# Performance work log

Hardware: AMD Instinct MI355X
Metric: run time of the kernel (lower is better)

Reference implementation:

```python
import jax, jax.numpy as jnp
import numpy as np

INPUT_DIM = 1024
BOTTLENECK = 256
NUM_Q = 8
CODEBOOK = 1024
COMMIT_W = 0.25

def setup_inputs() -> dict:
    key = jax.random.key(0)
    ks = jax.random.split(key, 10)
    s_in = 1.0 / np.sqrt(INPUT_DIM)
    s_bn = 1.0 / np.sqrt(BOTTLENECK)
    return {
        'x': jax.random.normal(ks[0], (8, 2048, INPUT_DIM), jnp.float32),
        'W_e1': jax.random.uniform(ks[1], (INPUT_DIM, INPUT_DIM), jnp.float32, -s_in, s_in),
        'b_e1': jnp.zeros((INPUT_DIM,), jnp.float32),
        'W_e2': jax.random.uniform(ks[2], (INPUT_DIM, BOTTLENECK), jnp.float32, -s_in, s_in),
        'b_e2': jnp.zeros((BOTTLENECK,), jnp.float32),
        'codebooks': jax.random.normal(ks[3], (NUM_Q, CODEBOOK, BOTTLENECK), jnp.float32),
        'W_d1': jax.random.uniform(ks[4], (BOTTLENECK, INPUT_DIM), jnp.float32, -s_bn, s_bn),
        'b_d1': jnp.zeros((INPUT_DIM,), jnp.float32),
        'W_d2': jax.random.uniform(ks[5], (INPUT_DIM, INPUT_DIM), jnp.float32, -s_in, s_in),
        'b_d2': jnp.zeros((INPUT_DIM,), jnp.float32),
    }

def _gelu(x):
    return jax.nn.gelu(x, approximate=False)  # torch nn.GELU default = exact erf

def _rvq(z_flat, codebooks):
    # z_flat: [N, D]; codebooks: [Q, K, D]
    def step(res, cb):
        # squared L2 distances via expansion: [N, K]
        d2 = (jnp.sum(res * res, -1, keepdims=True)
              - 2.0 * res @ cb.T
              + jnp.sum(cb * cb, -1))
        idx = jnp.argmin(d2, axis=-1)                      # [N]
        q = jax.lax.stop_gradient(jnp.take(cb, idx, 0))    # [N, D] (EMA codebook: no grad)
        closs = jnp.mean((res - q) ** 2)
        return res - q, (idx, q, closs)
    _, (indices, qs, closses) = jax.lax.scan(step, z_flat, codebooks)
    q_total = jnp.sum(qs, axis=0)
    # straight-through estimator
    quantized = z_flat + jax.lax.stop_gradient(q_total - z_flat)
    commitment = COMMIT_W * jnp.mean(closses)
    return quantized, indices, commitment

def reference(x, W_e1, b_e1, W_e2, b_e2, codebooks, W_d1, b_d1, W_d2, b_d2):
    lead = x.shape[:-1]
    z = _gelu(x @ W_e1 + b_e1) @ W_e2 + b_e2               # [..., BOTTLENECK]
    zf = z.reshape(-1, BOTTLENECK)
    qf, indices, commitment = _rvq(zf, codebooks)
    quantized = qf.reshape(*lead, BOTTLENECK)
    indices = indices.reshape(NUM_Q, *lead)
    reconstructed = _gelu(quantized @ W_d1 + b_d1) @ W_d2 + b_d2
    return z, quantized, indices, reconstructed, commitment
```

## Files before the change

### kernel.cpp

```cpp
#include <hip/hip_runtime.h>
#include <math.h>

#define NROWS 16384
#define DIN   1024
#define DBN   256
#define NQ    8
#define NCODE 1024
#define MARGIN 2.0f

#define OFF_Z    0
#define OFF_Q    4194304
#define OFF_IDX  8388608
#define OFF_REC  8519680
#define OFF_COM  25296896

typedef __attribute__((ext_vector_type(8))) short short8v;
typedef __attribute__((ext_vector_type(4))) float f32x4;

__device__ __forceinline__ float gelu_f(float x) {
  return 0.5f * x * (1.0f + erff(x * 0.70710678118654752440f));
}

__device__ __forceinline__ ushort f2b(float x) {
  unsigned u = __float_as_uint(x);
  unsigned r = u + 0x7FFF + ((u >> 16) & 1);
  return (ushort)(r >> 16);
}
__device__ __forceinline__ float b2f(ushort u) {
  return __uint_as_float((unsigned)u << 16);
}
__device__ __forceinline__ void split3(float v, ushort& s1, ushort& s2, ushort& s3) {
  s1 = f2b(v);
  const float r1 = v - b2f(s1);
  s2 = f2b(r1);
  const float r2 = r1 - b2f(s2);
  s3 = f2b(r2);
}

template<bool GELU, int NB, int OUT>
__global__ __launch_bounds__(256) void gemm6(
    const float* __restrict__ Af,
    const ushort* __restrict__ B1, const ushort* __restrict__ B2,
    const ushort* __restrict__ B3,
    const float* __restrict__ bias,
    float* __restrict__ C0, float* __restrict__ C1, ushort* __restrict__ Ob,
    int N, int K)
{
  constexpr int BN = NB * 32;
  __shared__ char lds[24576 + BN * 192];
  char* ldsA = lds;
  char* ldsB = lds + 24576;
  const int tid = threadIdx.x;
  const int bm = blockIdx.x * 128;
  const int bn = blockIdx.y * BN;
  const int lane = tid & 63;
  const int wid = tid >> 6;
  const int wr = wid >> 1, wc = wid & 1;

  const int srow = tid >> 1, skh = tid & 1;
  const float* Ap = Af + (size_t)(bm + srow) * K + skh * 16;
  const int abase = srow * 192;
  const int aswz = (srow & 7) << 4;

  f32x4 acc[4][NB];
  #pragma unroll
  for (int m = 0; m < 4; ++m)
    #pragma unroll
    for (int n = 0; n < NB; ++n) acc[m][n] = (f32x4)0.f;

  union U8 { ushort u[8]; short8v v; };

  const int nt = K >> 5;
  for (int t = 0; t < nt; ++t) {
    const int k0 = t << 5;
    __syncthreads();
    float av[16];
    *(float4*)&av[0]  = *(const float4*)(Ap + k0);
    *(float4*)&av[4]  = *(const float4*)(Ap + k0 + 4);
    *(float4*)&av[8]  = *(const float4*)(Ap + k0 + 8);
    *(float4*)&av[12] = *(const float4*)(Ap + k0 + 12);
    U8 p1[2], p2[2], p3[2];
    #pragma unroll
    for (int i = 0; i < 16; ++i) {
      ushort s1, s2, s3;
      split3(av[i], s1, s2, s3);
      p1[i >> 3].u[i & 7] = s1;
      p2[i >> 3].u[i & 7] = s2;
      p3[i >> 3].u[i & 7] = s3;
    }
    #pragma unroll
    for (int h2 = 0; h2 < 2; ++h2) {
      const int kb = skh * 32 + h2 * 16;
      *(short8v*)(ldsA + ((abase + 0   + kb) ^ aswz)) = p1[h2].v;
      *(short8v*)(ldsA + ((abase + 64  + kb) ^ aswz)) = p2[h2].v;
      *(short8v*)(ldsA + ((abase + 128 + kb) ^ aswz)) = p3[h2].v;
    }
    if (NB == 4) {
      const int br = tid >> 1, bk = tid & 1;
      const size_t g = (size_t)(bn + br) * K + k0 + bk * 16;
      const int bb = br * 192, bswz = (br & 7) << 4;
      #pragma unroll
      for (int h2 = 0; h2 < 2; ++h2) {
        const int kb = bk * 32 + h2 * 16;
        *(uint4*)(ldsB + ((bb + 0   + kb) ^ bswz)) = *(const uint4*)(B1 + g + h2 * 8);
        *(uint4*)(ldsB + ((bb + 64  + kb) ^ bswz)) = *(const uint4*)(B2 + g + h2 * 8);
        *(uint4*)(ldsB + ((bb + 128 + kb) ^ bswz)) = *(const uint4*)(B3 + g + h2 * 8);
      }
    } else {
      const int br = tid >> 2, bk = tid & 3;
      const size_t g = (size_t)(bn + br) * K + k0 + bk * 8;
      const int bb = br * 192, bswz = (br & 7) << 4;
      const int kb = bk * 16;
      *(uint4*)(ldsB + ((bb + 0   + kb) ^ bswz)) = *(const uint4*)(B1 + g);
      *(uint4*)(ldsB + ((bb + 64  + kb) ^ bswz)) = *(const uint4*)(B2 + g);
      *(uint4*)(ldsB + ((bb + 128 + kb) ^ bswz)) = *(const uint4*)(B3 + g);
    }
    __syncthreads();

    const int kq = (lane >> 4) << 4;
    short8v a1[4], a2[4], a3[4], b1v[NB], b2v[NB], b3v[NB];
    #pragma unroll
    for (int m = 0; m < 4; ++m) {
      const int row = wr * 64 + m * 16 + (lane & 15);
      const int base = row * 192, swz = (row & 7) << 4;
      a1[m] = *(const short8v*)(ldsA + ((base + 0   + kq) ^ swz));
      a2[m] = *(const short8v*)(ldsA + ((base + 64  + kq) ^ swz));
      a3[m] = *(const short8v*)(ldsA + ((base + 128 + kq) ^ swz));
    }
    #pragma unroll
    for (int n = 0; n < NB; ++n) {
      const int row = wc * (NB * 16) + n * 16 + (lane & 15);
      const int base = row * 192, swz = (row & 7) << 4;
      b1v[n] = *(const short8v*)(ldsB + ((base + 0   + kq) ^ swz));
      b2v[n] = *(const short8v*)(ldsB + ((base + 64  + kq) ^ swz));
      b3v[n] = *(const short8v*)(ldsB + ((base + 128 + kq) ^ swz));
    }
    #pragma unroll
    for (int m = 0; m < 4; ++m)
      #pragma unroll
      for (int n = 0; n < NB; ++n) {
        f32x4 a = acc[m][n];
        a = __builtin_amdgcn_mfma_f32_16x16x32_bf16(a3[m], b1v[n], a, 0, 0, 0);
        a = __builtin_amdgcn_mfma_f32_16x16x32_bf16(a1[m], b3v[n], a, 0, 0, 0);
        a = __builtin_amdgcn_mfma_f32_16x16x32_bf16(a2[m], b2v[n], a, 0, 0, 0);
        a = __builtin_amdgcn_mfma_f32_16x16x32_bf16(a2[m], b1v[n], a, 0, 0, 0);
        a = __builtin_amdgcn_mfma_f32_16x16x32_bf16(a1[m], b2v[n], a, 0, 0, 0);
        a = __builtin_amdgcn_mfma_f32_16x16x32_bf16(a1[m], b1v[n], a, 0, 0, 0);
        acc[m][n] = a;
      }
  }

  #pragma unroll
  for (int n = 0; n < NB; ++n) {
    const int col = bn + wc * (NB * 16) + n * 16 + (lane & 15);
    const float bb = bias[col];
    #pragma unroll
    for (int m = 0; m < 4; ++m) {
      const int row0 = bm + wr * 64 + m * 16 + ((lane >> 4) << 2);
      #pragma unroll
      for (int r = 0; r < 4; ++r) {
        float v = acc[m][n][r] + bb;
        if (GELU) v = gelu_f(v);
        C0[(size_t)(row0 + r) * N + col] = v;
        if (OUT == 1) {
          C1[(size_t)(row0 + r) * N + col] = v;
          Ob[(size_t)(row0 + r) * N + col] = f2b(v);
        }
      }
    }
  }
}

__device__ __forceinline__ void mm_core(
    const ushort* __restrict__ A, const ushort* __restrict__ B,
    int K, int bm, int bn, char* lds, f32x4 acc[4][4])
{
  char* ldsA = lds;
  char* ldsB = lds + 16384;
  const int tid = threadIdx.x;
  const int lane = tid & 63;
  const int wid = tid >> 6;
  const int wr = wid >> 1, wc = wid & 1;

  #pragma unroll
  for (int m = 0; m < 4; ++m)
    #pragma unroll
    for (int n = 0; n < 4; ++n) acc[m][n] = (f32x4)0.f;

  const int nt = K >> 6;
  for (int t = 0; t < nt; ++t) {
    const int k0 = t << 6;
    __syncthreads();
    #pragma unroll
    for (int c = 0; c < 4; ++c) {
      const int id = c * 256 + tid;
      const int row = id >> 3, k8 = id & 7;
      const uint4 va = *(const uint4*)(A + (size_t)(bm + row) * K + k0 + k8 * 8);
      const uint4 vb = *(const uint4*)(B + (size_t)(bn + row) * K + k0 + k8 * 8);
      const int off = (row * 128 + k8 * 16) ^ ((row & 7) << 4);
      *(uint4*)(ldsA + off) = va;
      *(uint4*)(ldsB + off) = vb;
    }
    __syncthreads();
    #pragma unroll
    for (int kk = 0; kk < 2; ++kk) {
      short8v af[4], bfr[4];
      #pragma unroll
      for (int m = 0; m < 4; ++m) {
        const int row = wr * 64 + m * 16 + (lane & 15);
        af[m] = *(const short8v*)(ldsA +
            ((row * 128 + kk * 64 + ((lane >> 4) << 4)) ^ ((row & 7) << 4)));
      }
      #pragma unroll
      for (int n = 0; n < 4; ++n) {
        const int row = wc * 64 + n * 16 + (lane & 15);
        bfr[n] = *(const short8v*)(ldsB +
            ((row * 128 + kk * 64 + ((lane >> 4) << 4)) ^ ((row & 7) << 4)));
      }
      #pragma unroll
      for (int m = 0; m < 4; ++m)
        #pragma unroll
        for (int n = 0; n < 4; ++n)
          acc[m][n] = __builtin_amdgcn_mfma_f32_16x16x32_bf16(
              af[m], bfr[n], acc[m][n], 0, 0, 0);
    }
  }
}

__global__ __launch_bounds__(256) void rvq_screen(
    const ushort* __restrict__ resb, const ushort* __restrict__ cbb,
    const float* __restrict__ cnorm, _Float16* __restrict__ D)
{
  __shared__ char lds[32768];
  f32x4 acc[4][4];
  const int bm = blockIdx.x * 128, bn = blockIdx.y * 128;
  mm_core(resb, cbb, DBN, bm, bn, lds, acc);
  const int lane = threadIdx.x & 63;
  const int wid = threadIdx.x >> 6;
  const int wr = wid >> 1, wc = wid & 1;
  #pragma unroll
  for (int n = 0; n < 4; ++n) {
    const int col = bn + wc * 64 + n * 16 + (lane & 15);
    const float cn = cnorm[col];
    #pragma unroll
    for (int m = 0; m < 4; ++m) {
      const int row0 = bm + wr * 64 + m * 16 + ((lane >> 4) << 2);
      #pragma unroll
      for (int r = 0; r < 4; ++r)
        D[(size_t)(row0 + r) * NCODE + col] = (_Float16)(cn - 2.0f * acc[m][n][r]);
    }
  }
}

template<bool GELU, bool OUTF>
__global__ __launch_bounds__(256) void gemm_bf16(
    const ushort* __restrict__ A, const ushort* __restrict__ Bt,
    const float* __restrict__ bias, float* __restrict__ Cf,
    ushort* __restrict__ Cb, int N, int K)
{
  __shared__ char lds[32768];
  f32x4 acc[4][4];
  const int bm = blockIdx.x * 128, bn = blockIdx.y * 128;
  mm_core(A, Bt, K, bm, bn, lds, acc);
  const int lane = threadIdx.x & 63;
  const int wid = threadIdx.x >> 6;
  const int wr = wid >> 1, wc = wid & 1;
  #pragma unroll
  for (int n = 0; n < 4; ++n) {
    const int col = bn + wc * 64 + n * 16 + (lane & 15);
    const float bb = bias[col];
    #pragma unroll
    for (int m = 0; m < 4; ++m) {
      const int row0 = bm + wr * 64 + m * 16 + ((lane >> 4) << 2);
      #pragma unroll
      for (int r = 0; r < 4; ++r) {
        float v = acc[m][n][r] + bb;
        if (GELU) v = gelu_f(v);
        if (OUTF) Cf[(size_t)(row0 + r) * N + col] = v;
        else      Cb[(size_t)(row0 + r) * N + col] = f2b(v);
      }
    }
  }
}

__global__ __launch_bounds__(256) void cnorm_kernel(
    const float* __restrict__ cb, float* __restrict__ cnorm)
{
  const int code = blockIdx.x * 4 + (threadIdx.x >> 6);
  const int lane = threadIdx.x & 63;
  float4 v = *(const float4*)(cb + (size_t)code * DBN + lane * 4);
  float s = v.x * v.x + v.y * v.y + v.z * v.z + v.w * v.w;
  #pragma unroll
  for (int o = 32; o > 0; o >>= 1) s += __shfl_down(s, o, 64);
  if (lane == 0) cnorm[code] = s;
}

__global__ __launch_bounds__(256) void rvq_rescore(
    const _Float16* __restrict__ D, const float* __restrict__ cb_s,
    const float* __restrict__ cnorm_s,
    float* __restrict__ res, ushort* __restrict__ resb,
    float* __restrict__ idx_out, float* __restrict__ closs_part)
{
  __shared__ int cnt[4];
  __shared__ ushort cand[4][128];
  __shared__ float wsum[4];
  const int w = threadIdx.x >> 6, lane = threadIdx.x & 63;
  const int row = blockIdx.x * 4 + w;
  if (lane == 0) cnt[w] = 0;

  union H8 { uint4 u; _Float16 h[8]; };
  const _Float16* Dr = D + (size_t)row * NCODE + lane * 16;
  H8 a0, a1;
  a0.u = *(const uint4*)(Dr);
  a1.u = *(const uint4*)(Dr + 8);
  float dv[16];
  #pragma unroll
  for (int i = 0; i < 8; ++i) { dv[i] = (float)a0.h[i]; dv[8 + i] = (float)a1.h[i]; }

  float mn = dv[0];
  #pragma unroll
  for (int i = 1; i < 16; ++i) mn = fminf(mn, dv[i]);
  #pragma unroll
  for (int o = 32; o > 0; o >>= 1) mn = fminf(mn, __shfl_xor(mn, o, 64));
  const float thr = mn + MARGIN;

  #pragma unroll
  for (int i = 0; i < 16; ++i)
    if (dv[i] < thr) {
      int p = atomicAdd(&cnt[w], 1);
      if (p < 128) cand[w][p] = (ushort)(lane * 16 + i);
    }
  const int ncand = min(cnt[w], 128);

  const float4 r4 = *(const float4*)(res + (size_t)row * DBN + lane * 4);
  float bestv = INFINITY; int besti = 0x7fffffff;
  for (int c = 0; c < ncand; ++c) {
    const int code = cand[w][c];
    const float4 c4 = *(const float4*)(cb_s + (size_t)code * DBN + lane * 4);
    float d = r4.x * c4.x + r4.y * c4.y + r4.z * c4.z + r4.w * c4.w;
    #pragma unroll
    for (int o = 32; o > 0; o >>= 1) d += __shfl_xor(d, o, 64);
    const float ex = cnorm_s[code] - 2.0f * d;
    if (ex < bestv || (ex == bestv && code < besti)) { bestv = ex; besti = code; }
  }

  const float4 q4 = *(const float4*)(cb_s + (size_t)besti * DBN + lane * 4);
  float4 n4;
  n4.x = r4.x - q4.x; n4.y = r4.y - q4.y; n4.z = r4.z - q4.z; n4.w = r4.w - q4.w;
  *(float4*)(res + (size_t)row * DBN + lane * 4) = n4;
  ushort4 nb;
  nb.x = f2b(n4.x); nb.y = f2b(n4.y); nb.z = f2b(n4.z); nb.w = f2b(n4.w);
  *(ushort4*)(resb + (size_t)row * DBN + lane * 4) = nb;

  float s = n4.x * n4.x + n4.y * n4.y + n4.z * n4.z + n4.w * n4.w;
  #pragma unroll
  for (int o = 32; o > 0; o >>= 1) s += __shfl_xor(s, o, 64);
  if (lane == 0) { wsum[w] = s; idx_out[row] = (float)besti; }
  __syncthreads();
  if (threadIdx.x == 0)
    closs_part[blockIdx.x] = wsum[0] + wsum[1] + wsum[2] + wsum[3];
}

__global__ __launch_bounds__(256) void qfix_gather(
    const float* __restrict__ z, const float* __restrict__ idxf,
    const float* __restrict__ cb, float* __restrict__ q, ushort* __restrict__ qb)
{
  const int w = threadIdx.x >> 6, lane = threadIdx.x & 63;
  const int row = blockIdx.x * 4 + w;
  float4 a; a.x = 0.f; a.y = 0.f; a.z = 0.f; a.w = 0.f;
  #pragma unroll
  for (int s = 0; s < NQ; ++s) {
    const int ix = (int)idxf[(size_t)s * NROWS + row];
    const float4 c4 = *(const float4*)(cb + ((size_t)s * NCODE + ix) * DBN + lane * 4);
    a.x += c4.x; a.y += c4.y; a.z += c4.z; a.w += c4.w;
  }
  const float4 z4 = *(const float4*)(z + (size_t)row * DBN + lane * 4);
  float4 qv;
  qv.x = z4.x + (a.x - z4.x); qv.y = z4.y + (a.y - z4.y);
  qv.z = z4.z + (a.z - z4.z); qv.w = z4.w + (a.w - z4.w);
  *(float4*)(q + (size_t)row * DBN + lane * 4) = qv;
  ushort4 qb4;
  qb4.x = f2b(qv.x); qb4.y = f2b(qv.y); qb4.z = f2b(qv.z); qb4.w = f2b(qv.w);
  *(ushort4*)(qb + (size_t)row * DBN + lane * 4) = qb4;
}

__global__ __launch_bounds__(256) void conv_flat(
    const float* __restrict__ in, ushort* __restrict__ out, int n4)
{
  const int i = blockIdx.x * 256 + threadIdx.x;
  if (i >= n4) return;
  const float4 v = *(const float4*)(in + (size_t)i * 4);
  ushort4 o;
  o.x = f2b(v.x); o.y = f2b(v.y); o.z = f2b(v.z); o.w = f2b(v.w);
  *(ushort4*)(out + (size_t)i * 4) = o;
}

__global__ __launch_bounds__(256) void convT(
    const float* __restrict__ in, ushort* __restrict__ out, int K, int N)
{
  __shared__ float t[32][33];
  const int k0 = blockIdx.x * 32, n0 = blockIdx.y * 32;
  const int tx = threadIdx.x & 31, ty = threadIdx.x >> 5;
  #pragma unroll
  for (int i = 0; i < 32; i += 8)
    t[ty + i][tx] = in[(size_t)(k0 + ty + i) * N + n0 + tx];
  __syncthreads();
  #pragma unroll
  for (int i = 0; i < 32; i += 8)
    out[(size_t)(n0 + ty + i) * K + k0 + tx] = f2b(t[tx][ty + i]);
}

__global__ __launch_bounds__(256) void convT_split3(
    const float* __restrict__ in, ushort* __restrict__ o1,
    ushort* __restrict__ o2, ushort* __restrict__ o3, int K, int N)
{
  __shared__ float t[32][33];
  const int k0 = blockIdx.x * 32, n0 = blockIdx.y * 32;
  const int tx = threadIdx.x & 31, ty = threadIdx.x >> 5;
  #pragma unroll
  for (int i = 0; i < 32; i += 8)
    t[ty + i][tx] = in[(size_t)(k0 + ty + i) * N + n0 + tx];
  __syncthreads();
  #pragma unroll
  for (int i = 0; i < 32; i += 8) {
    const float v = t[tx][ty + i];
    ushort s1, s2, s3;
    split3(v, s1, s2, s3);
    const size_t o = (size_t)(n0 + ty + i) * K + k0 + tx;
    o1[o] = s1; o2[o] = s2; o3[o] = s3;
  }
}

__global__ __launch_bounds__(256) void commit_kernel(
    const float* __restrict__ parts, float* __restrict__ out)
{
  __shared__ float sm[256];
  float s = 0.f;
  for (int i = threadIdx.x; i < NQ * 4096; i += 256) s += parts[i];
  sm[threadIdx.x] = s;
  __syncthreads();
  for (int st = 128; st > 0; st >>= 1) {
    if (threadIdx.x < st) sm[threadIdx.x] += sm[threadIdx.x + st];
    __syncthreads();
  }
  if (threadIdx.x == 0)
    out[0] = 0.25f * sm[0] / (8.0f * 4194304.0f);
}

extern "C" void kernel_launch(void* const* d_in, const int* in_sizes, int n_in,
                              void* d_out, int out_size, void* d_ws, size_t ws_size,
                              hipStream_t stream) {
  (void)in_sizes; (void)n_in; (void)out_size; (void)ws_size;
  const float* x    = (const float*)d_in[0];
  const float* W_e1 = (const float*)d_in[1];
  const float* b_e1 = (const float*)d_in[2];
  const float* W_e2 = (const float*)d_in[3];
  const float* b_e2 = (const float*)d_in[4];
  const float* cb   = (const float*)d_in[5];
  const float* W_d1 = (const float*)d_in[6];
  const float* b_d1 = (const float*)d_in[7];
  const float* W_d2 = (const float*)d_in[8];
  const float* b_d2 = (const float*)d_in[9];

  float* out = (float*)d_out;
  float* z_out   = out + OFF_Z;
  float* q_out   = out + OFF_Q;
  float* idx_out = out + OFF_IDX;
  float* rec_out = out + OFF_REC;
  float* com_out = out + OFF_COM;

  float* ws      = (float*)d_ws;
  float* hidden  = ws;
  float* res     = ws + 16777216;
  float* cnorm   = ws + 20971520;
  float* closs   = ws + 20979712;
  ushort* wtail  = (ushort*)(ws + 21012480);
  ushort* We2T1  = wtail;
  ushort* We2T2  = wtail + 262144;
  ushort* We2T3  = wtail + 524288;
  ushort* Wd1T   = wtail + 786432;
  ushort* Wd2T   = wtail + 1048576;

  ushort* resu   = (ushort*)res;
  ushort* We1T1  = resu;
  ushort* We1T2  = resu + 1048576;
  ushort* We1T3  = resu + 2097152;

  ushort* hregion = (ushort*)d_ws;
  _Float16* Dmat = (_Float16*)hregion;
  ushort* resb   = hregion + 16777216;
  ushort* cbb    = hregion + 20971520;
  ushort* qb     = hregion + 20971520;
  ushort* hidb   = hregion;

  cnorm_kernel<<<2048, 256, 0, stream>>>(cb, cnorm);
  convT_split3<<<dim3(32, 32), 256, 0, stream>>>(W_e1, We1T1, We1T2, We1T3, DIN, DIN);
  convT_split3<<<dim3(32, 8),  256, 0, stream>>>(W_e2, We2T1, We2T2, We2T3, DIN, DBN);
  convT<<<dim3(8, 32),  256, 0, stream>>>(W_d1, Wd1T, DBN, DIN);
  convT<<<dim3(32, 32), 256, 0, stream>>>(W_d2, Wd2T, DIN, DIN);

  gemm6<true,  4, 0><<<dim3(128, 8), 256, 0, stream>>>(
      x, We1T1, We1T2, We1T3, b_e1, hidden, nullptr, nullptr, DIN, DIN);
  gemm6<false, 2, 1><<<dim3(128, 4), 256, 0, stream>>>(
      hidden, We2T1, We2T2, We2T3, b_e2, z_out, res, resb, DBN, DIN);

  conv_flat<<<2048, 256, 0, stream>>>(cb, cbb, 524288);

  for (int s = 0; s < NQ; ++s) {
    rvq_screen<<<dim3(128, 8), 256, 0, stream>>>(
        resb, cbb + (size_t)s * NCODE * DBN, cnorm + s * NCODE, Dmat);
    rvq_rescore<<<4096, 256, 0, stream>>>(
        Dmat, cb + (size_t)s * NCODE * DBN, cnorm + s * NCODE,
        res, resb, idx_out + (size_t)s * NROWS, closs + s * 4096);
  }

  qfix_gather<<<4096, 256, 0, stream>>>(z_out, idx_out, cb, q_out, qb);

  gemm_bf16<true,  false><<<dim3(128, 8), 256, 0, stream>>>(qb, Wd1T, b_d1, nullptr, hidb, DIN, DBN);
  gemm_bf16<false, true ><<<dim3(128, 8), 256, 0, stream>>>(hidb, Wd2T, b_d2, rec_out, nullptr, DIN, DIN);

  commit_kernel<<<1, 256, 0, stream>>>(closs, com_out);
}
```

Before: 683.3 us.

## Load A operand straight into MFMA registers, skipping LDS staging

```diff
diff --git a/kernel.cpp b/kernel.cpp
--- a/kernel.cpp
+++ b/kernel.cpp
@@ -47,9 +47,7 @@
     int N, int K)
 {
   constexpr int BN = NB * 32;
-  __shared__ char lds[24576 + BN * 192];
-  char* ldsA = lds;
-  char* ldsB = lds + 24576;
+  __shared__ char ldsB[BN * 192];
   const int tid = threadIdx.x;
   const int bm = blockIdx.x * 128;
   const int bn = blockIdx.y * BN;
@@ -57,10 +55,19 @@
   const int wid = tid >> 6;
   const int wr = wid >> 1, wc = wid & 1;
 
-  const int srow = tid >> 1, skh = tid & 1;
-  const float* Ap = Af + (size_t)(bm + srow) * K + skh * 16;
-  const int abase = srow * 192;
-  const int aswz = (srow & 7) << 4;
+  const float* Am[4];
+  #pragma unroll
+  for (int m = 0; m < 4; ++m)
+    Am[m] = Af + (size_t)(bm + wr * 64 + m * 16 + (lane & 15)) * K + (lane >> 4) * 8;
+
+  const int brow = tid & (BN - 1);
+  const int bsel = (NB == 4) ? (tid >> 7) : (tid >> 6);
+  const int bkoff = bsel * (NB == 4 ? 16 : 8);
+  const ushort* Bp1 = B1 + (size_t)(bn + brow) * K + bkoff;
+  const ushort* Bp2 = B2 + (size_t)(bn + brow) * K + bkoff;
+  const ushort* Bp3 = B3 + (size_t)(bn + brow) * K + bkoff;
+  const int bswz = (brow & 7) << 4;
+  const int bb0 = brow * 192 + 2 * bkoff;
 
   f32x4 acc[4][NB];
   #pragma unroll
@@ -73,81 +80,52 @@
   const int nt = K >> 5;
   for (int t = 0; t < nt; ++t) {
     const int k0 = t << 5;
+    float av[4][8];
+    #pragma unroll
+    for (int m = 0; m < 4; ++m) {
+      *(float4*)&av[m][0] = *(const float4*)(Am[m] + k0);
+      *(float4*)&av[m][4] = *(const float4*)(Am[m] + k0 + 4);
+    }
     __syncthreads();
-    float av[16];
-    *(float4*)&av[0]  = *(const float4*)(Ap + k0);
-    *(float4*)&av[4]  = *(const float4*)(Ap + k0 + 4);
-    *(float4*)&av[8]  = *(const float4*)(Ap + k0 + 8);
-    *(float4*)&av[12] = *(const float4*)(Ap + k0 + 12);
-    U8 p1[2], p2[2], p3[2];
-    #pragma unroll
-    for (int i = 0; i < 16; ++i) {
-      ushort s1, s2, s3;
-      split3(av[i], s1, s2, s3);
-      p1[i >> 3].u[i & 7] = s1;
-      p2[i >> 3].u[i & 7] = s2;
-      p3[i >> 3].u[i & 7] = s3;
-    }
-    #pragma unroll
-    for (int h2 = 0; h2 < 2; ++h2) {
-      const int kb = skh * 32 + h2 * 16;
-      *(short8v*)(ldsA + ((abase + 0   + kb) ^ aswz)) = p1[h2].v;
-      *(short8v*)(ldsA + ((abase + 64  + kb) ^ aswz)) = p2[h2].v;
-      *(short8v*)(ldsA + ((abase + 128 + kb) ^ aswz)) = p3[h2].v;
-    }
     if (NB == 4) {
-      const int br = tid >> 1, bk = tid & 1;
-      const size_t g = (size_t)(bn + br) * K + k0 + bk * 16;
-      const int bb = br * 192, bswz = (br & 7) << 4;
       #pragma unroll
       for (int h2 = 0; h2 < 2; ++h2) {
-        const int kb = bk * 32 + h2 * 16;
-        *(uint4*)(ldsB + ((bb + 0   + kb) ^ bswz)) = *(const uint4*)(B1 + g + h2 * 8);
-        *(uint4*)(ldsB + ((bb + 64  + kb) ^ bswz)) = *(const uint4*)(B2 + g + h2 * 8);
-        *(uint4*)(ldsB + ((bb + 128 + kb) ^ bswz)) = *(const uint4*)(B3 + g + h2 * 8);
+        *(uint4*)(ldsB + ((bb0 + 0   + h2 * 16) ^ bswz)) = *(const uint4*)(Bp1 + k0 + h2 * 8);
+        *(uint4*)(ldsB + ((bb0 + 64  + h2 * 16) ^ bswz)) = *(const uint4*)(Bp2 + k0 + h2 * 8);
+        *(uint4*)(ldsB + ((bb0 + 128 + h2 * 16) ^ bswz)) = *(const uint4*)(Bp3 + k0 + h2 * 8);
       }
     } else {
-      const int br = tid >> 2, bk = tid & 3;
-      const size_t g = (size_t)(bn + br) * K + k0 + bk * 8;
-      const int bb = br * 192, bswz = (br & 7) << 4;
-      const int kb = bk * 16;
-      *(uint4*)(ldsB + ((bb + 0   + kb) ^ bswz)) = *(const uint4*)(B1 + g);
-      *(uint4*)(ldsB + ((bb + 64  + kb) ^ bswz)) = *(const uint4*)(B2 + g);
-      *(uint4*)(ldsB + ((bb + 128 + kb) ^ bswz)) = *(const uint4*)(B3 + g);
-    }
+      *(uint4*)(ldsB + ((bb0 + 0  ) ^ bswz)) = *(const uint4*)(Bp1 + k0);
+      *(uint4*)(ldsB + ((bb0 + 64 ) ^ bswz)) = *(const uint4*)(Bp2 + k0);
+      *(uint4*)(ldsB + ((bb0 + 128) ^ bswz)) = *(const uint4*)(Bp3 + k0);
+    }
+    U8 a1[4], a2[4], a3[4];
+    #pragma unroll
+    for (int m = 0; m < 4; ++m)
+      #pragma unroll
+      for (int i = 0; i < 8; ++i)
+        split3(av[m][i], a1[m].u[i], a2[m].u[i], a3[m].u[i]);
     __syncthreads();
-
     const int kq = (lane >> 4) << 4;
-    short8v a1[4], a2[4], a3[4], b1v[NB], b2v[NB], b3v[NB];
-    #pragma unroll
-    for (int m = 0; m < 4; ++m) {
-      const int row = wr * 64 + m * 16 + (lane & 15);
-      const int base = row * 192, swz = (row & 7) << 4;
-      a1[m] = *(const short8v*)(ldsA + ((base + 0   + kq) ^ swz));
-      a2[m] = *(const short8v*)(ldsA + ((base + 64  + kq) ^ swz));
-      a3[m] = *(const short8v*)(ldsA + ((base + 128 + kq) ^ swz));
-    }
     #pragma unroll
     for (int n = 0; n < NB; ++n) {
-      const int row = wc * (NB * 16) + n * 16 + (lane & 15);
-      const int base = row * 192, swz = (row & 7) << 4;
-      b1v[n] = *(const short8v*)(ldsB + ((base + 0   + kq) ^ swz));
-      b2v[n] = *(const short8v*)(ldsB + ((base + 64  + kq) ^ swz));
-      b3v[n] = *(const short8v*)(ldsB + ((base + 128 + kq) ^ swz));
-    }
-    #pragma unroll
-    for (int m = 0; m < 4; ++m)
-      #pragma unroll
-      for (int n = 0; n < NB; ++n) {
+      const int rowb = wc * (NB * 16) + n * 16 + (lane & 15);
+      const int base = rowb * 192, swz = (rowb & 7) << 4;
+      const short8v b1 = *(const short8v*)(ldsB + ((base + 0   + kq) ^ swz));
+      const short8v b2 = *(const short8v*)(ldsB + ((base + 64  + kq) ^ swz));
+      const short8v b3 = *(const short8v*)(ldsB + ((base + 128 + kq) ^ swz));
+      #pragma unroll
+      for (int m = 0; m < 4; ++m) {
         f32x4 a = acc[m][n];
-        a = __builtin_amdgcn_mfma_f32_16x16x32_bf16(a3[m], b1v[n], a, 0, 0, 0);
-        a = __builtin_amdgcn_mfma_f32_16x16x32_bf16(a1[m], b3v[n], a, 0, 0, 0);
-        a = __builtin_amdgcn_mfma_f32_16x16x32_bf16(a2[m], b2v[n], a, 0, 0, 0);
-        a = __builtin_amdgcn_mfma_f32_16x16x32_bf16(a2[m], b1v[n], a, 0, 0, 0);
-        a = __builtin_amdgcn_mfma_f32_16x16x32_bf16(a1[m], b2v[n], a, 0, 0, 0);
-        a = __builtin_amdgcn_mfma_f32_16x16x32_bf16(a1[m], b1v[n], a, 0, 0, 0);
+        a = __builtin_amdgcn_mfma_f32_16x16x32_bf16(a3[m].v, b1, a, 0, 0, 0);
+        a = __builtin_amdgcn_mfma_f32_16x16x32_bf16(a1[m].v, b3, a, 0, 0, 0);
+        a = __builtin_amdgcn_mfma_f32_16x16x32_bf16(a2[m].v, b2, a, 0, 0, 0);
+        a = __builtin_amdgcn_mfma_f32_16x16x32_bf16(a2[m].v, b1, a, 0, 0, 0);
+        a = __builtin_amdgcn_mfma_f32_16x16x32_bf16(a1[m].v, b2, a, 0, 0, 0);
+        a = __builtin_amdgcn_mfma_f32_16x16x32_bf16(a1[m].v, b1, a, 0, 0, 0);
         acc[m][n] = a;
       }
+    }
   }
 
   #pragma unroll
```

Result: slower. 971.4 us (+42.2%).
